# Kernel optimization log

Measured on AMD Instinct MI355X. Metric: run time of the kernel, lower is better.

## Reference

```python
import jax, jax.numpy as jnp
import numpy as np

DIM = 1024
HEADS = 16
DIM_HEAD = 64
INNER = HEADS * DIM_HEAD
SEQ = 4096
BATCH = 1


def setup_inputs() -> dict:
    key = jax.random.key(0)
    ks = jax.random.split(key, 6)
    s = 0.02
    return {
        "x": jax.random.normal(ks[0], (BATCH, SEQ, DIM), dtype=jnp.float32),
        "Wq": jax.random.normal(ks[1], (DIM, INNER), dtype=jnp.float32) * s,
        "Wk": jax.random.normal(ks[2], (DIM, INNER), dtype=jnp.float32) * s,
        "Wv": jax.random.normal(ks[3], (DIM, INNER), dtype=jnp.float32) * s,
        "Wo": jax.random.normal(ks[4], (INNER, DIM), dtype=jnp.float32) * s,
        "bo": jax.random.normal(ks[5], (DIM,), dtype=jnp.float32) * s,
    }


def reference(x, Wq, Wk, Wv, Wo, bo):
    b, n, _ = x.shape
    beta = 1.0 / jnp.sqrt(jnp.float32(DIM_HEAD))
    # project and split heads: [b, n, inner] -> [b, h, n, d]
    def split_heads(t):
        return t.reshape(b, n, HEADS, DIM_HEAD).transpose(0, 2, 1, 3)
    q = split_heads(x @ Wq)
    k = split_heads(x @ Wk)
    v = split_heads(x @ Wv)
    # scaled scores [b, h, n, n]
    scores = jnp.einsum('bhid,bhjd->bhij', q * beta, k)
    mask_value = -jnp.finfo(scores.dtype).max
    causal = jnp.triu(jnp.ones((n, n), dtype=bool), k=1)
    scores = jnp.where(causal, mask_value, scores)
    attn = jax.nn.softmax(scores, axis=-1)
    out = jnp.einsum('bhij,bhjd->bhid', attn, v)
    out = out.transpose(0, 2, 1, 3).reshape(b, n, INNER)
    # output projection (dropout is identity in eval)
    return out @ Wo + bo
```

## Files before the change

### kernel.cpp

```cpp
#include <hip/hip_runtime.h>
#include <hip/hip_bf16.h>
#include <stdint.h>
#include <math.h>

#define SEQ 4096
#define DIM 1024
#define NHEADS 16
#define DHEAD 64
#define INNER 1024

typedef __hip_bfloat16 bf16;
typedef __attribute__((ext_vector_type(8))) short short8;
typedef __attribute__((ext_vector_type(4))) float floatx4;

__device__ __forceinline__ void gll16(const bf16* g, bf16* l) {
    __builtin_amdgcn_global_load_lds(
        (const __attribute__((address_space(1))) unsigned int*)g,
        (__attribute__((address_space(3))) unsigned int*)l,
        16, 0, 0);
}

__device__ __forceinline__ unsigned short f2bf_bits(float f) {
    bf16 h = __float2bfloat16(f);
    return *reinterpret_cast<unsigned short*>(&h);
}

__device__ __forceinline__ uint2 pack4bf(float a, float b, float c, float d) {
    __hip_bfloat162 lo = __float22bfloat162_rn(float2{a, b});
    __hip_bfloat162 hi = __float22bfloat162_rn(float2{c, d});
    uint2 r;
    r.x = *reinterpret_cast<unsigned*>(&lo);
    r.y = *reinterpret_cast<unsigned*>(&hi);
    return r;
}

__global__ __launch_bounds__(256) void prep_kernel(
        const float* __restrict__ x, const float* __restrict__ W0,
        const float* __restrict__ W1, const float* __restrict__ W2,
        const float* __restrict__ W3, bf16* __restrict__ xb,
        bf16* __restrict__ T0, bf16* __restrict__ T1,
        bf16* __restrict__ T2, bf16* __restrict__ T3) {
    const int tid = threadIdx.x + threadIdx.y * blockDim.x;
    if (blockIdx.z == 4) {
        int chunk = blockIdx.y * 32 + blockIdx.x;
        int base = chunk * 4096 + tid * 4;
        #pragma unroll
        for (int r = 0; r < 4; r++) {
            int i = base + r * 1024;
            float4 f = *reinterpret_cast<const float4*>(x + i);
            unsigned long long p = (unsigned long long)f2bf_bits(f.x)
                                 | ((unsigned long long)f2bf_bits(f.y) << 16)
                                 | ((unsigned long long)f2bf_bits(f.z) << 32)
                                 | ((unsigned long long)f2bf_bits(f.w) << 48);
            *reinterpret_cast<unsigned long long*>(xb + i) = p;
        }
        return;
    }
    const float* W; bf16* T;
    switch (blockIdx.z) {
        case 0:  W = W0; T = T0; break;
        case 1:  W = W1; T = T1; break;
        case 2:  W = W2; T = T2; break;
        default: W = W3; T = T3; break;
    }
    __shared__ float tile[32][33];
    int k0 = blockIdx.x * 32, n0 = blockIdx.y * 32;
    int tx = threadIdx.x, ty = threadIdx.y;
    #pragma unroll
    for (int i = 0; i < 4; i++)
        tile[ty + 8 * i][tx] = W[(size_t)(k0 + ty + 8 * i) * 1024 + n0 + tx];
    __syncthreads();
    #pragma unroll
    for (int i = 0; i < 4; i++)
        T[(size_t)(n0 + ty + 8 * i) * 1024 + k0 + tx] = __float2bfloat16(tile[tx][ty + 8 * i]);
}

__device__ __forceinline__ void gemm128_body(const bf16* __restrict__ A,
                                             const bf16* __restrict__ Bt,
                                             int m0, int n0, floatx4 acc[4][4]) {
    __shared__ __align__(16) bf16 As[8192];
    __shared__ __align__(16) bf16 Bs[8192];
    const int tid = threadIdx.x;
    const int wave = tid >> 6;
    const int lane = tid & 63;
    const int l15 = lane & 15;
    const int quad = lane >> 4;

    #pragma unroll
    for (int i = 0; i < 4; i++)
        #pragma unroll
        for (int j = 0; j < 4; j++)
            acc[i][j] = (floatx4){0.f, 0.f, 0.f, 0.f};

    for (int k0 = 0; k0 < 1024; k0 += 64) {
        __syncthreads();
        #pragma unroll
        for (int j = 0; j < 4; j++) {
            int t = wave * 4 + j;
            int row = (t >> 1) * 16 + l15;
            int kb = (t & 1) * 32 + quad * 8;
            gll16(A + (size_t)(m0 + row) * 1024 + k0 + kb, &As[t * 512]);
            gll16(Bt + (size_t)(n0 + row) * 1024 + k0 + kb, &Bs[t * 512]);
        }
        __syncthreads();
        #pragma unroll
        for (int ks = 0; ks < 2; ks++) {
            short8 af[4], bfr[4];
            #pragma unroll
            for (int i = 0; i < 4; i++)
                af[i] = *reinterpret_cast<const short8*>(
                    &As[((((wave >> 1) * 4 + i) * 2 + ks) * 512) + lane * 8]);
            #pragma unroll
            for (int j = 0; j < 4; j++)
                bfr[j] = *reinterpret_cast<const short8*>(
                    &Bs[((((wave & 1) * 4 + j) * 2 + ks) * 512) + lane * 8]);
            #pragma unroll
            for (int i = 0; i < 4; i++)
                #pragma unroll
                for (int j = 0; j < 4; j++)
                    acc[i][j] = __builtin_amdgcn_mfma_f32_16x16x32_bf16(af[i], bfr[j], acc[i][j], 0, 0, 0);
        }
    }
}

__global__ __launch_bounds__(256) void qkv_gemm_kernel(
        const bf16* __restrict__ xb,
        const bf16* __restrict__ Wqt, const bf16* __restrict__ Wkt, const bf16* __restrict__ Wvt,
        bf16* __restrict__ Qh, bf16* __restrict__ Kh, bf16* __restrict__ Vt) {
    const bf16* Bt;
    if (blockIdx.z == 0)      Bt = Wqt;
    else if (blockIdx.z == 1) Bt = Wkt;
    else                      Bt = Wvt;
    int n0 = blockIdx.x * 128, m0 = blockIdx.y * 128;
    floatx4 acc[4][4];
    gemm128_body(xb, Bt, m0, n0, acc);

    const int tid = threadIdx.x, wave = tid >> 6, lane = tid & 63;
    const int l15 = lane & 15, quad = lane >> 4;
    const int wm = (wave >> 1) * 64, wn = (wave & 1) * 64;
    if (blockIdx.z == 2) {
        #pragma unroll
        for (int i = 0; i < 4; i++)
            #pragma unroll
            for (int j = 0; j < 4; j++) {
                int col = n0 + wn + j * 16 + l15;
                int h = col >> 6, d = col & 63;
                int row0 = m0 + wm + i * 16 + quad * 4;
                uint2 v = pack4bf(acc[i][j][0], acc[i][j][1], acc[i][j][2], acc[i][j][3]);
                *reinterpret_cast<uint2*>(Vt + ((size_t)h * DHEAD + d) * SEQ + row0) = v;
            }
    } else {
        bf16* O = (blockIdx.z == 0) ? Qh : Kh;
        float scale = (blockIdx.z == 0) ? 0.125f * 1.4426950408889634f : 1.0f;
        #pragma unroll
        for (int i = 0; i < 4; i++)
            #pragma unroll
            for (int j = 0; j < 4; j++) {
                int col = n0 + wn + j * 16 + l15;
                int h = col >> 6, d = col & 63;
                #pragma unroll
                for (int r = 0; r < 4; r++) {
                    int row = m0 + wm + i * 16 + quad * 4 + r;
                    O[((size_t)h * SEQ + row) * DHEAD + d] = __float2bfloat16(acc[i][j][r] * scale);
                }
            }
    }
}

__global__ __launch_bounds__(256) void out_gemm_kernel(
        const bf16* __restrict__ Oa, const bf16* __restrict__ Wot,
        const float* __restrict__ bo, float* __restrict__ out) {
    int n0 = blockIdx.x * 128, m0 = blockIdx.y * 128;
    floatx4 acc[4][4];
    gemm128_body(Oa, Wot, m0, n0, acc);

    const int tid = threadIdx.x, wave = tid >> 6, lane = tid & 63;
    const int l15 = lane & 15, quad = lane >> 4;
    const int wm = (wave >> 1) * 64, wn = (wave & 1) * 64;
    #pragma unroll
    for (int i = 0; i < 4; i++)
        #pragma unroll
        for (int j = 0; j < 4; j++) {
            int col = n0 + wn + j * 16 + l15;
            float b = bo[col];
            #pragma unroll
            for (int r = 0; r < 4; r++) {
                int row = m0 + wm + i * 16 + quad * 4 + r;
                out[(size_t)row * DIM + col] = acc[i][j][r] + b;
            }
        }
}

__global__ __launch_bounds__(256, 4) void attention_kernel(
        const bf16* __restrict__ Qh, const bf16* __restrict__ Kh,
        const bf16* __restrict__ Vt, bf16* __restrict__ Oa) {
    __shared__ __align__(16) bf16 Ksh[8192];
    __shared__ __align__(16) bf16 Vsh[8192];
    __shared__ __align__(16) bf16 Ps[4][2048];
    const int tid = threadIdx.x, wave = tid >> 6, lane = tid & 63;
    const int l15 = lane & 15, quad = lane >> 4;
    const int id = blockIdx.x;
    const int head = id & 15;
    const int qt = 63 - (id >> 4);
    const int qw = qt * 64 + wave * 16;
    const size_t hoff = (size_t)head * SEQ * DHEAD;
    const bf16* Qb = Qh + hoff;
    const bf16* Kb = Kh + hoff;
    const bf16* Vb = Vt + hoff;

    short8 bq[2];
    #pragma unroll
    for (int s = 0; s < 2; s++)
        bq[s] = *reinterpret_cast<const short8*>(
            Qb + (size_t)(qw + l15) * DHEAD + s * 32 + quad * 8);

    floatx4 acc_o[4];
    #pragma unroll
    for (int c = 0; c < 4; c++) acc_o[c] = (floatx4){0.f, 0.f, 0.f, 0.f};
    float l_part = 0.f;

    const int ntiles = (qt + 2) >> 1;
    for (int kt = 0; kt < ntiles; kt++) {
        const int kbase = kt * 128;
        __syncthreads();
        #pragma unroll
        for (int j = 0; j < 4; j++) {
            int t = wave * 4 + j;
            gll16(Kb + (size_t)(kbase + (t >> 1) * 16 + l15) * DHEAD + (t & 1) * 32 + quad * 8,
                  &Ksh[t * 512]);
            gll16(Vb + (size_t)((t >> 2) * 16 + l15) * SEQ + kbase + (t & 3) * 32 + quad * 8,
                  &Vsh[t * 512]);
        }
        __syncthreads();

        floatx4 st[8];
        #pragma unroll
        for (int c = 0; c < 8; c++) st[c] = (floatx4){0.f, 0.f, 0.f, 0.f};
        #pragma unroll
        for (int c = 0; c < 8; c++) {
            short8 ak0 = *reinterpret_cast<const short8*>(&Ksh[(c * 2 + 0) * 512 + lane * 8]);
            short8 ak1 = *reinterpret_cast<const short8*>(&Ksh[(c * 2 + 1) * 512 + lane * 8]);
            st[c] = __builtin_amdgcn_mfma_f32_16x16x32_bf16(ak0, bq[0], st[c], 0, 0, 0);
            st[c] = __builtin_amdgcn_mfma_f32_16x16x32_bf16(ak1, bq[1], st[c], 0, 0, 0);
        }
        if (kbase + 127 > qw) {
            int base0 = kbase + quad * 4 - qw - l15;
            #pragma unroll
            for (int c = 0; c < 8; c++) {
                int base = base0 + c * 16;
                #pragma unroll
                for (int r = 0; r < 4; r++)
                    if (base + r > 0) st[c][r] = -1e30f;
            }
        }
        #pragma unroll
        for (int c = 0; c < 8; c++) {
            float p0 = __builtin_amdgcn_exp2f(st[c][0]);
            float p1 = __builtin_amdgcn_exp2f(st[c][1]);
            float p2 = __builtin_amdgcn_exp2f(st[c][2]);
            float p3 = __builtin_amdgcn_exp2f(st[c][3]);
            l_part += (p0 + p1) + (p2 + p3);
            int elem = (c >> 1) * 512
                     + (l15 + 16 * ((c & 1) * 2 + (quad >> 1))) * 8 + (quad & 1) * 4;
            *reinterpret_cast<uint2*>(&Ps[wave][elem]) = pack4bf(p0, p1, p2, p3);
        }
        #pragma unroll
        for (int s = 0; s < 4; s++) {
            short8 bp = *reinterpret_cast<const short8*>(&Ps[wave][s * 512 + lane * 8]);
            #pragma unroll
            for (int c = 0; c < 4; c++) {
                short8 av = *reinterpret_cast<const short8*>(&Vsh[(c * 4 + s) * 512 + lane * 8]);
                acc_o[c] = __builtin_amdgcn_mfma_f32_16x16x32_bf16(av, bp, acc_o[c], 0, 0, 0);
            }
        }
    }
    float l = l_part;
    l += __shfl_xor(l, 16, 64);
    l += __shfl_xor(l, 32, 64);
    float rcp = 1.0f / l;
    const int q = qw + l15;
    #pragma unroll
    for (int c = 0; c < 4; c++) {
        uint2 v = pack4bf(acc_o[c][0] * rcp, acc_o[c][1] * rcp,
                          acc_o[c][2] * rcp, acc_o[c][3] * rcp);
        *reinterpret_cast<uint2*>(Oa + (size_t)q * INNER + head * DHEAD + c * 16 + quad * 4) = v;
    }
}

extern "C" void kernel_launch(void* const* d_in, const int* in_sizes, int n_in,
                              void* d_out, int out_size, void* d_ws, size_t ws_size,
                              hipStream_t stream) {
    const float* x  = (const float*)d_in[0];
    const float* Wq = (const float*)d_in[1];
    const float* Wk = (const float*)d_in[2];
    const float* Wv = (const float*)d_in[3];
    const float* Wo = (const float*)d_in[4];
    const float* bo = (const float*)d_in[5];
    float* out = (float*)d_out;

    char* ws = (char*)d_ws;
    size_t off = 0;
    bf16* xb  = (bf16*)(ws + off); off += (size_t)SEQ * DIM * 2;
    bf16* Wqt = (bf16*)(ws + off); off += (size_t)DIM * INNER * 2;
    bf16* Wkt = (bf16*)(ws + off); off += (size_t)DIM * INNER * 2;
    bf16* Wvt = (bf16*)(ws + off); off += (size_t)DIM * INNER * 2;
    bf16* Wot = (bf16*)(ws + off); off += (size_t)INNER * DIM * 2;
    bf16* Qh  = (bf16*)(ws + off); off += (size_t)NHEADS * SEQ * DHEAD * 2;
    bf16* Kh  = (bf16*)(ws + off); off += (size_t)NHEADS * SEQ * DHEAD * 2;
    bf16* Vtr = (bf16*)(ws + off); off += (size_t)NHEADS * DHEAD * SEQ * 2;
    bf16* Oa  = (bf16*)(ws + off); off += (size_t)SEQ * INNER * 2;

    prep_kernel<<<dim3(32, 32, 5), dim3(32, 8), 0, stream>>>(x, Wq, Wk, Wv, Wo,
                                                             xb, Wqt, Wkt, Wvt, Wot);
    qkv_gemm_kernel<<<dim3(8, 32, 3), 256, 0, stream>>>(xb, Wqt, Wkt, Wvt, Qh, Kh, Vtr);
    attention_kernel<<<1024, 256, 0, stream>>>(Qh, Kh, Vtr, Oa);
    out_gemm_kernel<<<dim3(8, 32), 256, 0, stream>>>(Oa, Wot, bo, out);
}
```

Measured before the change: 258.9 us.

## Double-buffer K/V tiles with 64-key tiles, balanced block order, and MFMA priority

Shrinks the attention key tile from 128 to 64 and double-buffers K/V in shared memory. The next tile is prefetched with global_load_lds while the current one is computed, so each iteration needs one barrier instead of two. Blocks are reordered so heavy and light causal query tiles interleave, and s_setprio raises wave priority around the MFMA sections. The smaller tiles mean more loop iterations and less masking waste, at the cost of a per-iteration barrier that depends on async load completion ordering.

```diff
diff --git a/kernel.cpp b/kernel.cpp
--- a/kernel.cpp
+++ b/kernel.cpp
@@ -194,14 +194,16 @@
 __global__ __launch_bounds__(256, 4) void attention_kernel(
         const bf16* __restrict__ Qh, const bf16* __restrict__ Kh,
         const bf16* __restrict__ Vt, bf16* __restrict__ Oa) {
-    __shared__ __align__(16) bf16 Ksh[8192];
-    __shared__ __align__(16) bf16 Vsh[8192];
-    __shared__ __align__(16) bf16 Ps[4][2048];
+    __shared__ __align__(16) bf16 Ksh[2][4096];
+    __shared__ __align__(16) bf16 Vsh[2][4096];
+    __shared__ __align__(16) bf16 Ps[4][1024];
     const int tid = threadIdx.x, wave = tid >> 6, lane = tid & 63;
     const int l15 = lane & 15, quad = lane >> 4;
     const int id = blockIdx.x;
     const int head = id & 15;
-    const int qt = 63 - (id >> 4);
+    const int rk = id >> 4;
+    const int r0 = rk & 15, bsel = (rk >> 4) & 1, c2 = rk >> 5;
+    const int qt = bsel ? (2 * r0 + c2) : (63 - 2 * r0 - c2);
     const int qw = qt * 64 + wave * 16;
     const size_t hoff = (size_t)head * SEQ * DHEAD;
     const bf16* Qb = Qh + hoff;
@@ -219,34 +221,41 @@
     for (int c = 0; c < 4; c++) acc_o[c] = (floatx4){0.f, 0.f, 0.f, 0.f};
     float l_part = 0.f;
 
-    const int ntiles = (qt + 2) >> 1;
+    auto stage = [&](int buf, int kbase) {
+        #pragma unroll
+        for (int j = 0; j < 2; j++) {
+            int t = wave * 2 + j;
+            gll16(Kb + (size_t)(kbase + (t >> 1) * 16 + l15) * DHEAD + (t & 1) * 32 + quad * 8,
+                  &Ksh[buf][t * 512]);
+            gll16(Vb + (size_t)((t >> 1) * 16 + l15) * SEQ + kbase + (t & 1) * 32 + quad * 8,
+                  &Vsh[buf][t * 512]);
+        }
+    };
+
+    const int ntiles = qt + 1;
+    stage(0, 0);
+    __syncthreads();
+    int cur = 0;
     for (int kt = 0; kt < ntiles; kt++) {
-        const int kbase = kt * 128;
-        __syncthreads();
-        #pragma unroll
-        for (int j = 0; j < 4; j++) {
-            int t = wave * 4 + j;
-            gll16(Kb + (size_t)(kbase + (t >> 1) * 16 + l15) * DHEAD + (t & 1) * 32 + quad * 8,
-                  &Ksh[t * 512]);
-            gll16(Vb + (size_t)((t >> 2) * 16 + l15) * SEQ + kbase + (t & 3) * 32 + quad * 8,
-                  &Vsh[t * 512]);
-        }
-        __syncthreads();
-
-        floatx4 st[8];
-        #pragma unroll
-        for (int c = 0; c < 8; c++) st[c] = (floatx4){0.f, 0.f, 0.f, 0.f};
-        #pragma unroll
-        for (int c = 0; c < 8; c++) {
-            short8 ak0 = *reinterpret_cast<const short8*>(&Ksh[(c * 2 + 0) * 512 + lane * 8]);
-            short8 ak1 = *reinterpret_cast<const short8*>(&Ksh[(c * 2 + 1) * 512 + lane * 8]);
+        const int kbase = kt * 64;
+        if (kt + 1 < ntiles) stage(cur ^ 1, (kt + 1) * 64);
+
+        floatx4 st[4];
+        #pragma unroll
+        for (int c = 0; c < 4; c++) st[c] = (floatx4){0.f, 0.f, 0.f, 0.f};
+        __builtin_amdgcn_s_setprio(1);
+        #pragma unroll
+        for (int c = 0; c < 4; c++) {
+            short8 ak0 = *reinterpret_cast<const short8*>(&Ksh[cur][(c * 2 + 0) * 512 + lane * 8]);
+            short8 ak1 = *reinterpret_cast<const short8*>(&Ksh[cur][(c * 2 + 1) * 512 + lane * 8]);
             st[c] = __builtin_amdgcn_mfma_f32_16x16x32_bf16(ak0, bq[0], st[c], 0, 0, 0);
             st[c] = __builtin_amdgcn_mfma_f32_16x16x32_bf16(ak1, bq[1], st[c], 0, 0, 0);
         }
-        if (kbase + 127 > qw) {
+        __builtin_amdgcn_s_setprio(0);
+        if (kbase + 63 > qw) {
             int base0 = kbase + quad * 4 - qw - l15;
             #pragma unroll
-            for (int c = 0; c < 8; c++) {
+            for (int c = 0; c < 4; c++) {
                 int base = base0 + c * 16;
                 #pragma unroll
                 for (int r = 0; r < 4; r++)
@@ -254,7 +263,7 @@
             }
         }
         #pragma unroll
-        for (int c = 0; c < 8; c++) {
+        for (int c = 0; c < 4; c++) {
             float p0 = __builtin_amdgcn_exp2f(st[c][0]);
             float p1 = __builtin_amdgcn_exp2f(st[c][1]);
             float p2 = __builtin_amdgcn_exp2f(st[c][2]);
@@ -264,15 +273,20 @@
                      + (l15 + 16 * ((c & 1) * 2 + (quad >> 1))) * 8 + (quad & 1) * 4;
             *reinterpret_cast<uint2*>(&Ps[wave][elem]) = pack4bf(p0, p1, p2, p3);
         }
-        #pragma unroll
-        for (int s = 0; s < 4; s++) {
+        __builtin_amdgcn_s_setprio(1);
+        #pragma unroll
+        for (int s = 0; s < 2; s++) {
             short8 bp = *reinterpret_cast<const short8*>(&Ps[wave][s * 512 + lane * 8]);
             #pragma unroll
             for (int c = 0; c < 4; c++) {
-                short8 av = *reinterpret_cast<const short8*>(&Vsh[(c * 4 + s) * 512 + lane * 8]);
+                short8 av = *reinterpret_cast<const short8*>(&Vsh[cur][(c * 2 + s) * 512 + lane * 8]);
                 acc_o[c] = __builtin_amdgcn_mfma_f32_16x16x32_bf16(av, bp, acc_o[c], 0, 0, 0);
             }
         }
+        __builtin_amdgcn_s_setprio(0);
+
+        __syncthreads();
+        cur ^= 1;
     }
     float l = l_part;
     l += __shfl_xor(l, 16, 64);
```

Measured after the change: 260.5 us. About the same (+0.6%).
